# Kernel optimization log

Measured on AMD Instinct MI355X. Metric: run time of the kernel, lower is better.

## Reference

```python
import jax, jax.numpy as jnp
import numpy as np

ITER_N = 3  # iterNum
DIM = 256   # channel dim entering MPNCOV
# static flat indices of the upper triangle (row-major of dim*dim), as in Triuvec
_TRIU_I, _TRIU_J = np.triu_indices(DIM)
TRIU_IDX = jnp.asarray(_TRIU_I * DIM + _TRIU_J)


def setup_inputs() -> dict:
    key = jax.random.key(0)
    x = jax.random.normal(key, (256, 256, 14, 14), dtype=jnp.float32)
    return {"x": x}


def reference(x):
    B, C, H, W = x.shape
    M = H * W
    xr = x.reshape(B, C, M)
    # Covpool: y = x @ I_hat @ x^T with I_hat = (1/M)(I - (1/M) 1 1^T)
    # equivalently (1/M) * centered Gram matrix
    xc = xr - xr.mean(axis=2, keepdims=True)
    cov = jnp.einsum('bcm,bdm->bcd', xc, xc) / M  # [B, C, C]
    # Sqrtm: Newton-Schulz iteration (iSQRT-COV)
    I = jnp.eye(C, dtype=x.dtype)
    normA = jnp.trace(cov, axis1=1, axis2=2)  # = (1/3)*sum(cov * 3I)
    A = cov / normA[:, None, None]
    ZY = 0.5 * (3.0 * I - A)
    Yk = jnp.matmul(A, ZY)
    Zk = ZY
    for _ in range(ITER_N - 2):
        ZY = 0.5 * (3.0 * I - jnp.matmul(Zk, Yk))
        Yk = jnp.matmul(Yk, ZY)
        Zk = jnp.matmul(ZY, Zk)
    YZY = 0.5 * jnp.matmul(Yk, 3.0 * I - jnp.matmul(Zk, Yk))
    y = YZY * jnp.sqrt(normA)[:, None, None]
    # Triuvec: extract upper-triangular entries, [B, C*(C+1)/2]
    return y.reshape(B, C * C)[:, TRIU_IDX]
```

## Files before the change

kernel.cpp:

```cpp
#include <hip/hip_runtime.h>
#include <math.h>

#define BB 256
#define CC 256
#define MN 196
#define TRI 32896

#define MSC 32.0f
#define INV_MSC  (1.0f/32.0f)
#define INV_MSC2 (1.0f/1024.0f)

typedef _Float16 f16;
typedef f16   f16x8 __attribute__((ext_vector_type(8)));
typedef float f32x4 __attribute__((ext_vector_type(4)));
typedef unsigned u32x4 __attribute__((ext_vector_type(4)));

__device__ __forceinline__ unsigned pack_split(float v) {
    f16 h = (f16)v;
    f16 l = (f16)(v - (float)h);
    return (unsigned)__builtin_bit_cast(unsigned short, h) |
           ((unsigned)__builtin_bit_cast(unsigned short, l) << 16);
}
__device__ __forceinline__ float unpack_split(unsigned w) {
    f16 h = __builtin_bit_cast(f16, (unsigned short)(w & 0xffffu));
    f16 l = __builtin_bit_cast(f16, (unsigned short)(w >> 16));
    return (float)h + (float)l;
}
__device__ __forceinline__ f16x8 swap_pairs(f16x8 v) {
    return __builtin_shufflevector(v, v, 1, 0, 3, 2, 5, 4, 7, 6);
}
__device__ __forceinline__ void gload_lds16(const unsigned* g, const f16* l) {
    __builtin_amdgcn_global_load_lds(
        (__attribute__((address_space(1))) void*)(size_t)g,
        (__attribute__((address_space(3))) void*)(unsigned)(size_t)l,
        16, 0, 0);
}

__global__ __launch_bounds__(256) void xsplit_kernel(const float* __restrict__ x,
                                                     float* __restrict__ vr,
                                                     unsigned* __restrict__ xs, int b0) {
    int wave = (blockIdx.x * 256 + threadIdx.x) >> 6;
    int lane = threadIdx.x & 63;
    int bl = wave >> 8;
    int c  = wave & 255;
    int bg = b0 + bl;
    const float* row = x + ((size_t)bg * CC + c) * MN;
    float a0 = row[lane], a1 = row[lane + 64], a2 = row[lane + 128];
    float a3 = (lane < MN - 192) ? row[lane + 192] : 0.0f;
    float s = a0 + a1 + a2 + a3;
    float q = a0 * a0 + a1 * a1 + a2 * a2 + a3 * a3;
    #pragma unroll
    for (int off = 32; off > 0; off >>= 1) {
        s += __shfl_xor(s, off, 64);
        q += __shfl_xor(q, off, 64);
    }
    float m = s * (1.0f / MN);
    if (lane == 0) vr[bg * CC + c] = q * (1.0f / MN) - m * m;
    unsigned* orow = xs + (size_t)bl * (CC * 224) + (size_t)c * 224;
    orow[lane]       = pack_split(MSC * (a0 - m));
    orow[lane + 64]  = pack_split(MSC * (a1 - m));
    orow[lane + 128] = pack_split(MSC * (a2 - m));
    if (lane < 4)       orow[lane + 192] = pack_split(MSC * (a3 - m));
    else if (lane < 32) orow[lane + 192] = 0u;
}

__global__ __launch_bounds__(256) void norm_kernel(const float* __restrict__ vr,
                                                   float* __restrict__ inv,
                                                   float* __restrict__ snorm,
                                                   float* __restrict__ invs, int b0) {
    __shared__ float red[256];
    int b = b0 + blockIdx.x, i = threadIdx.x;
    red[i] = vr[b * CC + i];
    __syncthreads();
    for (int s = 128; s > 0; s >>= 1) {
        if (i < s) red[i] += red[i + s];
        __syncthreads();
    }
    if (i == 0) {
        float n = red[0];
        inv[b] = 1.0f / n;
        float sq = sqrtf(n);
        snorm[b] = sq;
        invs[b] = 1.0f / sq;
    }
}

template <int MODE>
__global__ __launch_bounds__(512) void gemm512(const unsigned* __restrict__ Ag,
                                               const unsigned* __restrict__ Bg,
                                               const unsigned* __restrict__ Eg,
                                               void* __restrict__ Cg,
                                               const float alpha0, const float beta0,
                                               const float diag_add,
                                               const float* __restrict__ Sg, int b0) {
    constexpr int    LDK = (MODE == 2) ? 224 : 256;
    constexpr int    KCH = LDK / 32;
    constexpr size_t BST = (size_t)CC * LDK;
    __shared__ __align__(16) unsigned char smem[65536];
    f16* AsBuf = (f16*)smem;
    f16* BsBuf = (f16*)(smem + 32768);
    unsigned* tile = (unsigned*)smem;

    const int bl = blockIdx.x / 3;
    const int t  = blockIdx.x - 3 * bl;
    const int bg = b0 + bl;
    const int ti = (t == 2) ? 1 : 0;
    const int tj = (t == 0) ? 0 : 1;
    const int tid  = threadIdx.x;
    const int lane = tid & 63;
    const int wid  = tid >> 6;
    const int wrow = wid >> 2, wcol = wid & 3;

    const unsigned* Abase = Ag + (size_t)bl * BST + (size_t)(ti * 128) * LDK;
    const unsigned* Bbase = Bg + (size_t)bl * BST + (size_t)(tj * 128) * LDK;

    const int sw = wid & 3;
    const unsigned* gsrc = (wid < 4) ? Abase : Bbase;
    const unsigned* gsl = gsrc + (size_t)(sw * 32 + (lane >> 3)) * LDK
                               + (((lane & 7) ^ ((lane >> 3) & 7)) << 2);
    f16* mbase = (wid < 4) ? AsBuf : BsBuf;

    int aoff[4][2], boff[2][2];
    #pragma unroll
    for (int ib = 0; ib < 4; ++ib) {
        int r = wrow * 64 + ib * 16 + (lane & 15);
        #pragma unroll
        for (int tt = 0; tt < 2; ++tt)
            aoff[ib][tt] = r * 128 + ((((tt * 4) + (lane >> 4)) ^ (r & 7)) << 4);
    }
    #pragma unroll
    for (int jb = 0; jb < 2; ++jb) {
        int r = wcol * 32 + jb * 16 + (lane & 15);
        #pragma unroll
        for (int tt = 0; tt < 2; ++tt)
            boff[jb][tt] = r * 128 + ((((tt * 4) + (lane >> 4)) ^ (r & 7)) << 4);
    }

    f32x4 acc[4][2];
    #pragma unroll
    for (int i = 0; i < 4; ++i)
        #pragma unroll
        for (int j = 0; j < 2; ++j) acc[i][j] = 0.0f;

    auto STAGE = [&](int nb, int ks) {
        const unsigned* s = gsl + (size_t)ks * 32;
        f16* d = mbase + nb * 8192 + sw * 2048;
        #pragma unroll
        for (int i = 0; i < 4; ++i)
            gload_lds16(s + (size_t)i * 8 * LDK, d + i * 512);
    };

    STAGE(0, 0);
    __syncthreads();
    #pragma unroll 1
    for (int ks = 0; ks < KCH; ++ks) {
        const int nb = ks & 1;
        if (ks + 1 < KCH) STAGE(nb ^ 1, ks + 1);
        const char* Ab8 = (const char*)(AsBuf + nb * 8192);
        const char* Bb8 = (const char*)(BsBuf + nb * 8192);
        #pragma unroll
        for (int tt = 0; tt < 2; ++tt) {
            f16x8 av[4], bv[2], bw[2];
            #pragma unroll
            for (int ib = 0; ib < 4; ++ib)
                av[ib] = *(const f16x8*)(Ab8 + aoff[ib][tt]);
            #pragma unroll
            for (int jb = 0; jb < 2; ++jb) {
                bv[jb] = *(const f16x8*)(Bb8 + boff[jb][tt]);
                bw[jb] = swap_pairs(bv[jb]);
            }
            #pragma unroll
            for (int ib = 0; ib < 4; ++ib)
                #pragma unroll
                for (int jb = 0; jb < 2; ++jb) {
                    acc[ib][jb] = __builtin_amdgcn_mfma_f32_16x16x32_f16(av[ib], bv[jb], acc[ib][jb], 0, 0, 0);
                    acc[ib][jb] = __builtin_amdgcn_mfma_f32_16x16x32_f16(av[ib], bw[jb], acc[ib][jb], 0, 0, 0);
                }
        }
        __syncthreads();
    }

    const int li0 = wrow * 64 + ((lane >> 4) << 2);
    const int lj  = wcol * 32 + (lane & 15);
    const int gi0base = ti * 128 + li0;
    const int gjbase  = tj * 128 + lj;

    if (MODE != 1) {
        float sc = (Sg != nullptr) ? Sg[bg] : 1.0f;
        float al = alpha0 * sc;
        float be = beta0 * sc;
        unsigned* Cb = (unsigned*)Cg + (size_t)bl * CC * CC;
        const unsigned* Eb = (Eg != nullptr) ? Eg + (size_t)bl * CC * CC : nullptr;

        if (Eb) {
            #pragma unroll
            for (int it = 0; it < 8; ++it) {
                int g = it * 512 + tid;
                int r = g >> 5, c4 = g & 31;
                *(u32x4*)&tile[r * 128 + c4 * 4] =
                    *(const u32x4*)&Eb[(size_t)(ti * 128 + r) * CC + tj * 128 + c4 * 4];
            }
            __syncthreads();
        }

        unsigned pk[4][2][4];
        #pragma unroll
        for (int ib = 0; ib < 4; ++ib)
            #pragma unroll
            for (int jb = 0; jb < 2; ++jb)
                #pragma unroll
                for (int q = 0; q < 4; ++q) {
                    int lr = li0 + q + 16 * ib;
                    int lc = lj + 16 * jb;
                    float val = al * acc[ib][jb][q];
                    if (Eb) val += be * unpack_split(tile[lr * 128 + lc]);
                    if (gi0base + q + 16 * ib == gjbase + 16 * jb) val += diag_add;
                    pk[ib][jb][q] = pack_split(val);
                }
        __syncthreads();

        #pragma unroll
        for (int ib = 0; ib < 4; ++ib)
            #pragma unroll
            for (int jb = 0; jb < 2; ++jb)
                #pragma unroll
                for (int q = 0; q < 4; ++q)
                    tile[(li0 + q + 16 * ib) * 128 + lj + 16 * jb] = pk[ib][jb][q];
        __syncthreads();

        #pragma unroll
        for (int it = 0; it < 8; ++it) {
            int g = it * 512 + tid;
            int r = g >> 5, c4 = g & 31;
            *(u32x4*)&Cb[(size_t)(ti * 128 + r) * CC + tj * 128 + c4 * 4] =
                *(const u32x4*)&tile[r * 128 + c4 * 4];
        }
        if (ti != tj) {
            #pragma unroll
            for (int ib = 0; ib < 4; ++ib)
                #pragma unroll
                for (int jb = 0; jb < 2; ++jb) {
                    int gj  = gjbase + 16 * jb;
                    int gi0 = gi0base + 16 * ib;
                    u32x4 m = {pk[ib][jb][0], pk[ib][jb][1], pk[ib][jb][2], pk[ib][jb][3]};
                    *(u32x4*)&Cb[(size_t)gj * CC + gi0] = m;
                }
        }
    } else {
        float* ob = (float*)Cg + (size_t)bg * TRI;
        #pragma unroll
        for (int ib = 0; ib < 4; ++ib)
            #pragma unroll
            for (int jb = 0; jb < 2; ++jb) {
                int gi0 = gi0base + ib * 16;
                int gj  = gjbase + jb * 16;
                #pragma unroll
                for (int q = 0; q < 4; ++q) {
                    int gi = gi0 + q;
                    if (gj >= gi)
                        ob[gi * CC - (gi * (gi - 1)) / 2 - gi + gj] = acc[ib][jb][q] * INV_MSC2;
                }
            }
    }
}

extern "C" void kernel_launch(void* const* d_in, const int* in_sizes, int n_in,
                              void* d_out, int out_size, void* d_ws, size_t ws_size,
                              hipStream_t stream) {
    const float* x = (const float*)d_in[0];
    float* out = (float*)d_out;
    unsigned* ws = (unsigned*)d_ws;

    const int SCR = BB * CC + 3 * BB;
    float* vr    = out + (out_size - SCR);
    float* inv   = vr + BB * CC;
    float* snorm = inv + BB;
    float* invs  = snorm + BB;

    size_t per_b = 4ull * CC * CC * sizeof(unsigned);
    int gmax = (int)(ws_size / per_b);
    int g = 1;
    while (g * 2 <= gmax && g * 2 <= BB) g *= 2;

    size_t slotf = (size_t)g * CC * CC;
    unsigned* s0 = ws;
    unsigned* s1 = ws + slotf;
    unsigned* s2 = ws + 2 * slotf;
    unsigned* s3 = ws + 3 * slotf;

    for (int b0 = 0; b0 < BB; b0 += g) {
        xsplit_kernel<<<g * 64, 256, 0, stream>>>(x, vr, s1, b0);
        norm_kernel<<<g, 256, 0, stream>>>(vr, inv, snorm, invs, b0);
        gemm512<2><<<g * 3, 512, 0, stream>>>(s1, s1, nullptr, (void*)s0,
                                              1.0f / (MSC * MN), 0.0f, 0.0f, inv, b0);
        gemm512<0><<<g * 3, 512, 0, stream>>>(s0, s0, s0, (void*)s1, -0.5f * INV_MSC, 1.5f, 0.0f, nullptr, b0);
        gemm512<0><<<g * 3, 512, 0, stream>>>(s0, s1, s1, (void*)s2, 0.25f * INV_MSC, -0.75f, 1.5f * MSC, nullptr, b0);
        gemm512<0><<<g * 3, 512, 0, stream>>>(s1, s2, nullptr, (void*)s3, INV_MSC, 0.0f, 0.0f, snorm, b0);
        gemm512<0><<<g * 3, 512, 0, stream>>>(s2, s0, s2, (void*)s1, -0.5f * INV_MSC, 1.5f, 0.0f, invs, b0);
        gemm512<0><<<g * 3, 512, 0, stream>>>(s1, s3, nullptr, (void*)s0, -0.5f * INV_MSC, 0.0f, 1.5f * MSC, nullptr, b0);
        gemm512<1><<<g * 3, 512, 0, stream>>>(s3, s0, nullptr, d_out, 0.0f, 0.0f, 0.0f, nullptr, b0);
    }
}
```

Baseline: 433.6 us.

## Compute all four 128x128 tiles with 256-thread blocks and XCD-aware block remap

Replaces the 512-thread GEMM, which computed only three symmetric tiles and mirrored the off-diagonal one, with a 256-thread GEMM that computes all four 128x128 output tiles. Each wave now covers a 64x64 sub-tile, giving more MFMA work per LDS fragment read. Block indices are remapped so consecutive blocks of one batch land on the same XCD, and the covariance K dimension is padded to 256. The cost is a third more MFMA work per matrix and extra padded K work in the first GEMM, in exchange for simpler stores and better register reuse.

Measured after the change: 400.1 us. -7.7%, faster.

```diff
diff --git a/kernel.cpp b/kernel.cpp
--- a/kernel.cpp
+++ b/kernel.cpp
@@ -56,12 +56,11 @@
     }
     float m = s * (1.0f / MN);
     if (lane == 0) vr[bg * CC + c] = q * (1.0f / MN) - m * m;
-    unsigned* orow = xs + (size_t)bl * (CC * 224) + (size_t)c * 224;
+    unsigned* orow = xs + ((size_t)bl * CC + c) * 256;
     orow[lane]       = pack_split(MSC * (a0 - m));
     orow[lane + 64]  = pack_split(MSC * (a1 - m));
     orow[lane + 128] = pack_split(MSC * (a2 - m));
-    if (lane < 4)       orow[lane + 192] = pack_split(MSC * (a3 - m));
-    else if (lane < 32) orow[lane + 192] = 0u;
+    orow[lane + 192] = (lane < 4) ? pack_split(MSC * (a3 - m)) : 0u;
 }
 
 __global__ __launch_bounds__(256) void norm_kernel(const float* __restrict__ vr,
@@ -85,94 +84,83 @@
     }
 }
 
-template <int MODE>
-__global__ __launch_bounds__(512) void gemm512(const unsigned* __restrict__ Ag,
+template <bool FINAL>
+__global__ __launch_bounds__(256) void gemm256(const unsigned* __restrict__ Ag,
                                                const unsigned* __restrict__ Bg,
                                                const unsigned* __restrict__ Eg,
                                                void* __restrict__ Cg,
                                                const float alpha0, const float beta0,
                                                const float diag_add,
                                                const float* __restrict__ Sg, int b0) {
-    constexpr int    LDK = (MODE == 2) ? 224 : 256;
-    constexpr int    KCH = LDK / 32;
-    constexpr size_t BST = (size_t)CC * LDK;
     __shared__ __align__(16) unsigned char smem[65536];
-    f16* AsBuf = (f16*)smem;
-    f16* BsBuf = (f16*)(smem + 32768);
-    unsigned* tile = (unsigned*)smem;
-
-    const int bl = blockIdx.x / 3;
-    const int t  = blockIdx.x - 3 * bl;
+
+    int bid = blockIdx.x;
+    const int nwg = gridDim.x;
+    if ((nwg & 7) == 0) {
+        const int cpx = nwg >> 3;
+        bid = (bid & 7) * cpx + (bid >> 3);
+    }
+    const int bl = bid >> 2;
+    const int t  = bid & 3;
+    const int ti = t >> 1, tj = t & 1;
+    if (FINAL && ti == 1 && tj == 0) return;
     const int bg = b0 + bl;
-    const int ti = (t == 2) ? 1 : 0;
-    const int tj = (t == 0) ? 0 : 1;
     const int tid  = threadIdx.x;
     const int lane = tid & 63;
     const int wid  = tid >> 6;
-    const int wrow = wid >> 2, wcol = wid & 3;
-
-    const unsigned* Abase = Ag + (size_t)bl * BST + (size_t)(ti * 128) * LDK;
-    const unsigned* Bbase = Bg + (size_t)bl * BST + (size_t)(tj * 128) * LDK;
-
-    const int sw = wid & 3;
-    const unsigned* gsrc = (wid < 4) ? Abase : Bbase;
-    const unsigned* gsl = gsrc + (size_t)(sw * 32 + (lane >> 3)) * LDK
-                               + (((lane & 7) ^ ((lane >> 3) & 7)) << 2);
-    f16* mbase = (wid < 4) ? AsBuf : BsBuf;
-
-    int aoff[4][2], boff[2][2];
-    #pragma unroll
-    for (int ib = 0; ib < 4; ++ib) {
-        int r = wrow * 64 + ib * 16 + (lane & 15);
-        #pragma unroll
-        for (int tt = 0; tt < 2; ++tt)
-            aoff[ib][tt] = r * 128 + ((((tt * 4) + (lane >> 4)) ^ (r & 7)) << 4);
-    }
-    #pragma unroll
-    for (int jb = 0; jb < 2; ++jb) {
-        int r = wcol * 32 + jb * 16 + (lane & 15);
-        #pragma unroll
-        for (int tt = 0; tt < 2; ++tt)
-            boff[jb][tt] = r * 128 + ((((tt * 4) + (lane >> 4)) ^ (r & 7)) << 4);
-    }
-
-    f32x4 acc[4][2];
+    const int wr = wid >> 1, wc = wid & 1;
+    const int h = lane >> 4;
+    const int d = lane & 15;
+
+    const unsigned* Abase = Ag + (size_t)bl * (CC * CC) + (size_t)(ti * 128) * 256;
+    const unsigned* Bbase = Bg + (size_t)bl * (CC * CC) + (size_t)(tj * 128) * 256;
+
+    const unsigned* gpan = (wid < 2) ? Abase : Bbase;
+    f16* lpan = (f16*)(smem + ((wid < 2) ? 0 : 32768));
+    const int rbase = (wid & 1) * 64;
+    const int sr = lane >> 3;
+    const int sg = (lane & 7) ^ (lane >> 3);
+
+    auto STAGE = [&](int nb, int ks) {
+        #pragma unroll
+        for (int i = 0; i < 8; ++i) {
+            const unsigned* src = gpan + (size_t)(rbase + i * 8 + sr) * 256
+                                       + ks * 32 + sg * 4;
+            f16* dst = lpan + nb * 8192 + (rbase + i * 8) * 64;
+            gload_lds16(src, dst);
+        }
+    };
+
+    f32x4 acc[4][4];
     #pragma unroll
     for (int i = 0; i < 4; ++i)
         #pragma unroll
-        for (int j = 0; j < 2; ++j) acc[i][j] = 0.0f;
-
-    auto STAGE = [&](int nb, int ks) {
-        const unsigned* s = gsl + (size_t)ks * 32;
-        f16* d = mbase + nb * 8192 + sw * 2048;
-        #pragma unroll
-        for (int i = 0; i < 4; ++i)
-            gload_lds16(s + (size_t)i * 8 * LDK, d + i * 512);
-    };
+        for (int j = 0; j < 4; ++j) acc[i][j] = 0.0f;
 
     STAGE(0, 0);
     __syncthreads();
     #pragma unroll 1
-    for (int ks = 0; ks < KCH; ++ks) {
+    for (int ks = 0; ks < 8; ++ks) {
         const int nb = ks & 1;
-        if (ks + 1 < KCH) STAGE(nb ^ 1, ks + 1);
-        const char* Ab8 = (const char*)(AsBuf + nb * 8192);
-        const char* Bb8 = (const char*)(BsBuf + nb * 8192);
-        #pragma unroll
-        for (int tt = 0; tt < 2; ++tt) {
-            f16x8 av[4], bv[2], bw[2];
+        if (ks < 7) STAGE(nb ^ 1, ks + 1);
+        #pragma unroll
+        for (int kk = 0; kk < 2; ++kk) {
+            const int swz = (((kk * 4 + h) ^ (d & 7)) << 4);
+            f16x8 av[4], bv[4], bw[4];
             #pragma unroll
             for (int ib = 0; ib < 4; ++ib)
-                av[ib] = *(const f16x8*)(Ab8 + aoff[ib][tt]);
-            #pragma unroll
-            for (int jb = 0; jb < 2; ++jb) {
-                bv[jb] = *(const f16x8*)(Bb8 + boff[jb][tt]);
+                av[ib] = *(const f16x8*)(smem + nb * 16384
+                            + (wr * 64 + ib * 16 + d) * 128 + swz);
+            #pragma unroll
+            for (int jb = 0; jb < 4; ++jb) {
+                bv[jb] = *(const f16x8*)(smem + 32768 + nb * 16384
+                            + (wc * 64 + jb * 16 + d) * 128 + swz);
                 bw[jb] = swap_pairs(bv[jb]);
             }
             #pragma unroll
             for (int ib = 0; ib < 4; ++ib)
                 #pragma unroll
-                for (int jb = 0; jb < 2; ++jb) {
+                for (int jb = 0; jb < 4; ++jb) {
                     acc[ib][jb] = __builtin_amdgcn_mfma_f32_16x16x32_f16(av[ib], bv[jb], acc[ib][jb], 0, 0, 0);
                     acc[ib][jb] = __builtin_amdgcn_mfma_f32_16x16x32_f16(av[ib], bw[jb], acc[ib][jb], 0, 0, 0);
                 }
@@ -180,41 +168,42 @@
         __syncthreads();
     }
 
-    const int li0 = wrow * 64 + ((lane >> 4) << 2);
-    const int lj  = wcol * 32 + (lane & 15);
-    const int gi0base = ti * 128 + li0;
-    const int gjbase  = tj * 128 + lj;
-
-    if (MODE != 1) {
-        float sc = (Sg != nullptr) ? Sg[bg] : 1.0f;
-        float al = alpha0 * sc;
-        float be = beta0 * sc;
+    const int li0 = wr * 64 + h * 4;
+    const int lj0 = wc * 64 + d;
+    const int gi0 = ti * 128 + li0;
+    const int gj0 = tj * 128 + lj0;
+    unsigned* tile = (unsigned*)smem;
+
+    if (!FINAL) {
+        const float sc = (Sg != nullptr) ? Sg[bg] : 1.0f;
+        const float al = alpha0 * sc;
+        const float be = beta0 * sc;
         unsigned* Cb = (unsigned*)Cg + (size_t)bl * CC * CC;
         const unsigned* Eb = (Eg != nullptr) ? Eg + (size_t)bl * CC * CC : nullptr;
 
         if (Eb) {
             #pragma unroll
-            for (int it = 0; it < 8; ++it) {
-                int g = it * 512 + tid;
-                int r = g >> 5, c4 = g & 31;
+            for (int it = 0; it < 16; ++it) {
+                int f = it * 256 + tid;
+                int r = f >> 5, c4 = f & 31;
                 *(u32x4*)&tile[r * 128 + c4 * 4] =
                     *(const u32x4*)&Eb[(size_t)(ti * 128 + r) * CC + tj * 128 + c4 * 4];
             }
             __syncthreads();
         }
 
-        unsigned pk[4][2][4];
+        unsigned pk[4][4][4];
         #pragma unroll
         for (int ib = 0; ib < 4; ++ib)
             #pragma unroll
-            for (int jb = 0; jb < 2; ++jb)
+            for (int jb = 0; jb < 4; ++jb)
                 #pragma unroll
                 for (int q = 0; q < 4; ++q) {
-                    int lr = li0 + q + 16 * ib;
-                    int lc = lj + 16 * jb;
+                    int lr = li0 + ib * 16 + q;
+                    int lc = lj0 + jb * 16;
                     float val = al * acc[ib][jb][q];
                     if (Eb) val += be * unpack_split(tile[lr * 128 + lc]);
-                    if (gi0base + q + 16 * ib == gjbase + 16 * jb) val += diag_add;
+                    if (gi0 + ib * 16 + q == gj0 + jb * 16) val += diag_add;
                     pk[ib][jb][q] = pack_split(val);
                 }
         __syncthreads();
@@ -222,41 +211,30 @@
         #pragma unroll
         for (int ib = 0; ib < 4; ++ib)
             #pragma unroll
-            for (int jb = 0; jb < 2; ++jb)
+            for (int jb = 0; jb < 4; ++jb)
                 #pragma unroll
                 for (int q = 0; q < 4; ++q)
-                    tile[(li0 + q + 16 * ib) * 128 + lj + 16 * jb] = pk[ib][jb][q];
-        __syncthreads();
-
-        #pragma unroll
-        for (int it = 0; it < 8; ++it) {
-            int g = it * 512 + tid;
-            int r = g >> 5, c4 = g & 31;
+                    tile[(li0 + ib * 16 + q) * 128 + lj0 + jb * 16] = pk[ib][jb][q];
+        __syncthreads();
+
+        #pragma unroll
+        for (int it = 0; it < 16; ++it) {
+            int f = it * 256 + tid;
+            int r = f >> 5, c4 = f & 31;
             *(u32x4*)&Cb[(size_t)(ti * 128 + r) * CC + tj * 128 + c4 * 4] =
                 *(const u32x4*)&tile[r * 128 + c4 * 4];
         }
-        if (ti != tj) {
-            #pragma unroll
-            for (int ib = 0; ib < 4; ++ib)
-                #pragma unroll
-                for (int jb = 0; jb < 2; ++jb) {
-                    int gj  = gjbase + 16 * jb;
-                    int gi0 = gi0base + 16 * ib;
-                    u32x4 m = {pk[ib][jb][0], pk[ib][jb][1], pk[ib][jb][2], pk[ib][jb][3]};
-                    *(u32x4*)&Cb[(size_t)gj * CC + gi0] = m;
-                }
-        }
     } else {
         float* ob = (float*)Cg + (size_t)bg * TRI;
         #pragma unroll
         for (int ib = 0; ib < 4; ++ib)
             #pragma unroll
-            for (int jb = 0; jb < 2; ++jb) {
-                int gi0 = gi0base + ib * 16;
-                int gj  = gjbase + jb * 16;
+            for (int jb = 0; jb < 4; ++jb) {
+                int gib = gi0 + ib * 16;
+                int gj  = gj0 + jb * 16;
                 #pragma unroll
                 for (int q = 0; q < 4; ++q) {
-                    int gi = gi0 + q;
+                    int gi = gib + q;
                     if (gj >= gi)
                         ob[gi * CC - (gi * (gi - 1)) / 2 - gi + gj] = acc[ib][jb][q] * INV_MSC2;
                 }
@@ -291,13 +269,13 @@
     for (int b0 = 0; b0 < BB; b0 += g) {
         xsplit_kernel<<<g * 64, 256, 0, stream>>>(x, vr, s1, b0);
         norm_kernel<<<g, 256, 0, stream>>>(vr, inv, snorm, invs, b0);
-        gemm512<2><<<g * 3, 512, 0, stream>>>(s1, s1, nullptr, (void*)s0,
-                                              1.0f / (MSC * MN), 0.0f, 0.0f, inv, b0);
-        gemm512<0><<<g * 3, 512, 0, stream>>>(s0, s0, s0, (void*)s1, -0.5f * INV_MSC, 1.5f, 0.0f, nullptr, b0);
-        gemm512<0><<<g * 3, 512, 0, stream>>>(s0, s1, s1, (void*)s2, 0.25f * INV_MSC, -0.75f, 1.5f * MSC, nullptr, b0);
-        gemm512<0><<<g * 3, 512, 0, stream>>>(s1, s2, nullptr, (void*)s3, INV_MSC, 0.0f, 0.0f, snorm, b0);
-        gemm512<0><<<g * 3, 512, 0, stream>>>(s2, s0, s2, (void*)s1, -0.5f * INV_MSC, 1.5f, 0.0f, invs, b0);
-        gemm512<0><<<g * 3, 512, 0, stream>>>(s1, s3, nullptr, (void*)s0, -0.5f * INV_MSC, 0.0f, 1.5f * MSC, nullptr, b0);
-        gemm512<1><<<g * 3, 512, 0, stream>>>(s3, s0, nullptr, d_out, 0.0f, 0.0f, 0.0f, nullptr, b0);
-    }
-}
+        gemm256<false><<<g * 4, 256, 0, stream>>>(s1, s1, nullptr, (void*)s0,
+                                                  1.0f / (MSC * MN), 0.0f, 0.0f, inv, b0);
+        gemm256<false><<<g * 4, 256, 0, stream>>>(s0, s0, s0, (void*)s1, -0.5f * INV_MSC, 1.5f, 0.0f, nullptr, b0);
+        gemm256<false><<<g * 4, 256, 0, stream>>>(s0, s1, s1, (void*)s2, 0.25f * INV_MSC, -0.75f, 1.5f * MSC, nullptr, b0);
+        gemm256<false><<<g * 4, 256, 0, stream>>>(s1, s2, nullptr, (void*)s3, INV_MSC, 0.0f, 0.0f, snorm, b0);
+        gemm256<false><<<g * 4, 256, 0, stream>>>(s2, s0, s2, (void*)s1, -0.5f * INV_MSC, 1.5f, 0.0f, invs, b0);
+        gemm256<false><<<g * 4, 256, 0, stream>>>(s1, s3, nullptr, (void*)s0, -0.5f * INV_MSC, 0.0f, 1.5f * MSC, nullptr, b0);
+        gemm256<true><<<g * 4, 256, 0, stream>>>(s3, s0, nullptr, d_out, 0.0f, 0.0f, 0.0f, nullptr, b0);
+    }
+}
```
